# Optimization experiments

Hardware: AMD Instinct MI355X
Metric: run time of the kernel (lower is better)

## Reference

```python
import jax, jax.numpy as jnp
import numpy as np

D_MODEL = 1024
BATCH = 4
SEQ = 4096


def setup_inputs() -> dict:
    key = jax.random.key(0)
    kx, kq, kk, kv = jax.random.split(key, 4)
    x = jax.random.normal(kx, (BATCH, SEQ, D_MODEL), dtype=jnp.float32)
    s = 1.0 / np.sqrt(D_MODEL)
    w_q = jax.random.normal(kq, (D_MODEL, D_MODEL), dtype=jnp.float32) * s
    w_k = jax.random.normal(kk, (D_MODEL, D_MODEL), dtype=jnp.float32) * s
    w_v = jax.random.normal(kv, (D_MODEL, D_MODEL), dtype=jnp.float32) * s
    # causal mask: 1 = keep, 0 = masked out (matches torch masked_fill(mask==0, -inf))
    mask = jnp.tril(jnp.ones((SEQ, SEQ), dtype=jnp.int32))
    return {"x": x, "w_q": w_q, "w_k": w_k, "w_v": w_v, "mask": mask}


def reference(x, w_q, w_k, w_v, mask):
    # torch nn.Linear: y = x @ W^T
    q = jnp.einsum("bsd,ed->bse", x, w_q)
    k = jnp.einsum("bsd,ed->bse", x, w_k)
    v = jnp.einsum("bsd,ed->bse", x, w_v)
    scale = 1.0 / jnp.sqrt(jnp.asarray(q.shape[-1], dtype=q.dtype))
    scores = jnp.einsum("bqd,bkd->bqk", q, k) * scale  # [B, S, S]
    scores = jnp.where(mask == 0, -jnp.inf, scores)
    attn = jax.nn.softmax(scores, axis=-1)
    return jnp.einsum("bqk,bkd->bqd", attn, v)
```

## Files before the change

### kernel.cpp

```cpp
#include <hip/hip_runtime.h>
#include <stdint.h>


#define DM   1024
#define SEQ  4096
#define NB   4
#define MTOT (NB * SEQ)

typedef unsigned short u16;
typedef unsigned int u32;
typedef __bf16 bf16x8 __attribute__((ext_vector_type(8)));
typedef float f32x4 __attribute__((ext_vector_type(4)));

__device__ __forceinline__ u16 f2bf(float f) {
    u32 u = __float_as_uint(f);
    u32 r = (u + 0x7fffu + ((u >> 16) & 1u)) >> 16;
    return (u16)r;
}

__device__ __forceinline__ void gl_lds16(const void* gptr, void* lptr) {
    __builtin_amdgcn_global_load_lds(
        (const __attribute__((address_space(1))) void*)gptr,
        (__attribute__((address_space(3))) void*)lptr,
        16, 0, 0);
}

__global__ void cvt_kernel(const float* __restrict__ in, u16* __restrict__ out, int n8) {
    int i = blockIdx.x * 256 + threadIdx.x;
    if (i >= n8) return;
    const float4* p = (const float4*)in + (size_t)i * 2;
    float4 a = p[0], b = p[1];
    uint4 o;
    o.x = (u32)f2bf(a.x) | ((u32)f2bf(a.y) << 16);
    o.y = (u32)f2bf(a.z) | ((u32)f2bf(a.w) << 16);
    o.z = (u32)f2bf(b.x) | ((u32)f2bf(b.y) << 16);
    o.w = (u32)f2bf(b.z) | ((u32)f2bf(b.w) << 16);
    ((uint4*)out)[i] = o;
}

__global__ void zero_kernel(float* __restrict__ p, int n) {
    int i = blockIdx.x * 256 + threadIdx.x;
    if (i < n) p[i] = 0.f;
}

__device__ __forceinline__ void gemm_core(
    const u16* __restrict__ A, int lda,
    const u16* __restrict__ B, int ldb,
    int m0, int n0, int kend,
    u16* sA, u16* sB, f32x4 acc[4][4])
{
    const int tid  = threadIdx.x;
    const int lane = tid & 63;
    const int w    = tid >> 6;
    const int wr   = w >> 1, wc = w & 1;
    const int gi   = lane >> 4, fr = lane & 15;
    const int srow = lane >> 2;
    const int scol = (lane & 3) * 8;

    for (int kt = 0; kt < kend; kt += 32) {
#pragma unroll
        for (int r = 0; r < 2; ++r) {
            int c   = w * 2 + r;
            int row = c * 16 + srow;
            gl_lds16(A + (size_t)(m0 + row) * lda + kt + scol, sA + c * 512 + lane * 8);
            gl_lds16(B + (size_t)(n0 + row) * ldb + kt + scol, sB + c * 512 + lane * 8);
        }
        __syncthreads();
        bf16x8 af[4], bq[4];
#pragma unroll
        for (int mi = 0; mi < 4; ++mi)
            af[mi] = *(const bf16x8*)(sA + (wr * 64 + mi * 16 + fr) * 32 + gi * 8);
#pragma unroll
        for (int ni = 0; ni < 4; ++ni)
            bq[ni] = *(const bf16x8*)(sB + (wc * 64 + ni * 16 + fr) * 32 + gi * 8);
#pragma unroll
        for (int mi = 0; mi < 4; ++mi)
#pragma unroll
            for (int ni = 0; ni < 4; ++ni)
                acc[mi][ni] = __builtin_amdgcn_mfma_f32_16x16x32_bf16(
                    af[mi], bq[ni], acc[mi][ni], 0, 0, 0);
        __syncthreads();
    }
}

__global__ __launch_bounds__(256) void qkv_kernel(
    const u16* __restrict__ xb,
    const u16* __restrict__ wq, const u16* __restrict__ wk, const u16* __restrict__ wv,
    u16* __restrict__ Q, u16* __restrict__ K, u16* __restrict__ Vt)
{
    __shared__ __align__(16) u16 sA[128 * 32];
    __shared__ __align__(16) u16 sB[128 * 32];
    const int nt = blockIdx.x;
    const int mt = blockIdx.y;
    const int which = blockIdx.z;
    const u16* W = which == 0 ? wq : which == 1 ? wk : wv;

    f32x4 acc[4][4];
#pragma unroll
    for (int a = 0; a < 4; ++a)
#pragma unroll
        for (int b = 0; b < 4; ++b) acc[a][b] = f32x4{0.f, 0.f, 0.f, 0.f};

    gemm_core(xb, DM, W, DM, mt * 128, nt * 128, DM, sA, sB, acc);

    const int lane = threadIdx.x & 63;
    const int w = threadIdx.x >> 6, wr = w >> 1, wc = w & 1;
    const int gi = lane >> 4, fr = lane & 15;

    if (which < 2) {
        u16* O = which == 0 ? Q : K;
#pragma unroll
        for (int mi = 0; mi < 4; ++mi)
#pragma unroll
            for (int ni = 0; ni < 4; ++ni)
#pragma unroll
                for (int i = 0; i < 4; ++i) {
                    int gm = mt * 128 + wr * 64 + mi * 16 + gi * 4 + i;
                    int gn = nt * 128 + wc * 64 + ni * 16 + fr;
                    O[(size_t)gm * DM + gn] = f2bf(acc[mi][ni][i]);
                }
    } else {
#pragma unroll
        for (int mi = 0; mi < 4; ++mi)
#pragma unroll
            for (int ni = 0; ni < 4; ++ni) {
                int gm = mt * 128 + wr * 64 + mi * 16 + gi * 4;
                int gn = nt * 128 + wc * 64 + ni * 16 + fr;
                int b = gm >> 12, s = gm & (SEQ - 1);
                uint2 pk;
                pk.x = (u32)f2bf(acc[mi][ni][0]) | ((u32)f2bf(acc[mi][ni][1]) << 16);
                pk.y = (u32)f2bf(acc[mi][ni][2]) | ((u32)f2bf(acc[mi][ni][3]) << 16);
                *(uint2*)(Vt + ((size_t)(b * DM + gn)) * SEQ + s) = pk;
            }
    }
}

__global__ __launch_bounds__(256) void scores_kernel(
    const u16* __restrict__ Q, const u16* __restrict__ K,
    u16* __restrict__ P, float* __restrict__ rowsum, int b0)
{
    const int ktile = blockIdx.x, qtile = blockIdx.y, z = blockIdx.z;
    if (ktile > qtile) return;
    const int b = b0 + z;
    const u16* Qb = Q + (size_t)b * SEQ * DM;
    const u16* Kb = K + (size_t)b * SEQ * DM;
    u16* Pb = P + (size_t)z * SEQ * SEQ;

    __shared__ __align__(16) u16 sA[128 * 32];
    __shared__ __align__(16) u16 sB[128 * 32];
    f32x4 acc[4][4];
#pragma unroll
    for (int a = 0; a < 4; ++a)
#pragma unroll
        for (int c = 0; c < 4; ++c) acc[a][c] = f32x4{0.f, 0.f, 0.f, 0.f};

    gemm_core(Qb, DM, Kb, DM, qtile * 128, ktile * 128, DM, sA, sB, acc);

    const int lane = threadIdx.x & 63;
    const int w = threadIdx.x >> 6, wr = w >> 1, wc = w & 1;
    const int gi = lane >> 4, fr = lane & 15;
    const int qt0 = qtile * 128, kt0 = ktile * 128;

#pragma unroll
    for (int mi = 0; mi < 4; ++mi) {
        float rs[4] = {0.f, 0.f, 0.f, 0.f};
#pragma unroll
        for (int ni = 0; ni < 4; ++ni)
#pragma unroll
            for (int i = 0; i < 4; ++i) {
                int gq = qt0 + wr * 64 + mi * 16 + gi * 4 + i;
                int gk = kt0 + wc * 64 + ni * 16 + fr;
                float p = (gk <= gq) ? __expf(acc[mi][ni][i] * 0.03125f) : 0.f;
                Pb[(size_t)gq * SEQ + gk] = f2bf(p);
                rs[i] += p;
            }
#pragma unroll
        for (int i = 0; i < 4; ++i) {
            float s = rs[i];
            s += __shfl_xor(s, 1);
            s += __shfl_xor(s, 2);
            s += __shfl_xor(s, 4);
            s += __shfl_xor(s, 8);
            if (fr == 0) {
                int gq = qt0 + wr * 64 + mi * 16 + gi * 4 + i;
                atomicAdd(&rowsum[(size_t)b * SEQ + gq], s);
            }
        }
    }
}

__global__ __launch_bounds__(256) void pv_kernel(
    const u16* __restrict__ P, const u16* __restrict__ Vt,
    const float* __restrict__ rowsum, float* __restrict__ out, int b0)
{
    const int et = blockIdx.x;
    const int qt = 31 - (int)blockIdx.y;
    const int z = blockIdx.z;
    const int b = b0 + z;
    const u16* Pb = P + (size_t)z * SEQ * SEQ;
    const u16* Vb = Vt + (size_t)b * DM * SEQ;

    __shared__ __align__(16) u16 sA[128 * 32];
    __shared__ __align__(16) u16 sB[128 * 32];
    f32x4 acc[4][4];
#pragma unroll
    for (int a = 0; a < 4; ++a)
#pragma unroll
        for (int c = 0; c < 4; ++c) acc[a][c] = f32x4{0.f, 0.f, 0.f, 0.f};

    const int kend = (qt + 1) * 128;
    gemm_core(Pb, SEQ, Vb, SEQ, qt * 128, et * 128, kend, sA, sB, acc);

    const int lane = threadIdx.x & 63;
    const int w = threadIdx.x >> 6, wr = w >> 1, wc = w & 1;
    const int gi = lane >> 4, fr = lane & 15;

#pragma unroll
    for (int mi = 0; mi < 4; ++mi)
#pragma unroll
        for (int i = 0; i < 4; ++i) {
            int gq = qt * 128 + wr * 64 + mi * 16 + gi * 4 + i;
            float inv = 1.0f / rowsum[(size_t)b * SEQ + gq];
#pragma unroll
            for (int ni = 0; ni < 4; ++ni) {
                int ge = et * 128 + wc * 64 + ni * 16 + fr;
                out[((size_t)b * SEQ + gq) * DM + ge] = acc[mi][ni][i] * inv;
            }
        }
}

extern "C" void kernel_launch(void* const* d_in, const int* in_sizes, int n_in,
                              void* d_out, int out_size, void* d_ws, size_t ws_size,
                              hipStream_t stream)
{
    const float* x  = (const float*)d_in[0];
    const float* wq = (const float*)d_in[1];
    const float* wk = (const float*)d_in[2];
    const float* wv = (const float*)d_in[3];
    float* out = (float*)d_out;
    char* ws = (char*)d_ws;
    const size_t MB = 1u << 20;

    auto need = [&](int g) {
        return (size_t)(32 * g + 96 + 6) * MB + (size_t)(NB * SEQ * 4) + 65536;
    };
    int g = (ws_size >= need(4)) ? 4 : (ws_size >= need(2)) ? 2 : 1;

    size_t off = 0;
    u16* P  = (u16*)(ws);            off += (size_t)32 * MB * g;
    u16* xb = (u16*)(ws);
    u16* Q  = (u16*)(ws + off);      off += 32 * MB;
    u16* K  = (u16*)(ws + off);      off += 32 * MB;
    u16* Vt = (u16*)(ws + off);      off += 32 * MB;
    u16* wqb = (u16*)(ws + off);     off += 2 * MB;
    u16* wkb = (u16*)(ws + off);     off += 2 * MB;
    u16* wvb = (u16*)(ws + off);     off += 2 * MB;
    float* rowsum = (float*)(ws + off);

    cvt_kernel<<<(MTOT * DM / 8) / 256, 256, 0, stream>>>(x, xb, MTOT * DM / 8);
    cvt_kernel<<<(DM * DM / 8) / 256, 256, 0, stream>>>(wq, wqb, DM * DM / 8);
    cvt_kernel<<<(DM * DM / 8) / 256, 256, 0, stream>>>(wk, wkb, DM * DM / 8);
    cvt_kernel<<<(DM * DM / 8) / 256, 256, 0, stream>>>(wv, wvb, DM * DM / 8);
    zero_kernel<<<(NB * SEQ) / 256, 256, 0, stream>>>(rowsum, NB * SEQ);

    qkv_kernel<<<dim3(8, 128, 3), 256, 0, stream>>>(xb, wqb, wkb, wvb, Q, K, Vt);

    for (int b0 = 0; b0 < NB; b0 += g) {
        scores_kernel<<<dim3(32, 32, g), 256, 0, stream>>>(Q, K, P, rowsum, b0);
        pv_kernel<<<dim3(8, 32, g), 256, 0, stream>>>(P, Vt, rowsum, out, b0);
    }
}
```

Before: 604.3 us.

## Use 128x256 triple-buffered GEMM tiles, triangular scores grid, split-K PV with combine

Replaces the 128x128 single-buffered GEMM core with a 512-thread 128x256 tile, triple-buffered LDS staging with XOR swizzle, and fine-grained vmcnt waits instead of double syncthreads per k-step. The scores kernel now launches only lower-triangular tiles via a linear index, and the PV kernel splits the longest causal rows into two K halves through a balanced item table, with a combine kernel to sum and normalize. The goal is better data reuse, load/compute overlap, and load balance across the causal triangle. It costs an extra 32MB workspace buffer and a combine pass, plus more LDS per block.

```diff
diff --git a/kernel.cpp b/kernel.cpp
--- a/kernel.cpp
+++ b/kernel.cpp
@@ -6,6 +6,9 @@
 #define SEQ  4096
 #define NB   4
 #define MTOT (NB * SEQ)
+
+#define SLOT_U16 12288
+#define LDS_U16  36864
 
 typedef unsigned short u16;
 typedef unsigned int u32;
@@ -43,68 +46,87 @@
     if (i < n) p[i] = 0.f;
 }
 
-__device__ __forceinline__ void gemm_core(
-    const u16* __restrict__ A, int lda,
-    const u16* __restrict__ B, int ldb,
-    int m0, int n0, int kend,
-    u16* sA, u16* sB, f32x4 acc[4][4])
-{
+__device__ __forceinline__ void stage_tile(const u16* __restrict__ A, int lda, int m0,
+                                           const u16* __restrict__ B, int ldb, int n0,
+                                           int kt, u16* slot, int tid) {
+    int row  = tid >> 2;
+    int csrc = (((tid & 3) ^ (row & 3)) << 3);
+    gl_lds16(A + (size_t)(m0 + row) * lda + kt * 32 + csrc,       slot + tid * 8);
+    gl_lds16(B + (size_t)(n0 + row) * ldb + kt * 32 + csrc,       slot + 4096 + tid * 8);
+    gl_lds16(B + (size_t)(n0 + 128 + row) * ldb + kt * 32 + csrc, slot + 8192 + tid * 8);
+}
+
+__device__ __forceinline__ void gemm128x256(const u16* __restrict__ A, int lda,
+                                            const u16* __restrict__ B, int ldb,
+                                            int m0, int n0, int NT,
+                                            u16* lds, f32x4 acc[4][4]) {
     const int tid  = threadIdx.x;
     const int lane = tid & 63;
     const int w    = tid >> 6;
-    const int wr   = w >> 1, wc = w & 1;
+    const int wr   = w >> 2, wc = w & 3;
     const int gi   = lane >> 4, fr = lane & 15;
-    const int srow = lane >> 2;
-    const int scol = (lane & 3) * 8;
-
-    for (int kt = 0; kt < kend; kt += 32) {
-#pragma unroll
-        for (int r = 0; r < 2; ++r) {
-            int c   = w * 2 + r;
-            int row = c * 16 + srow;
-            gl_lds16(A + (size_t)(m0 + row) * lda + kt + scol, sA + c * 512 + lane * 8);
-            gl_lds16(B + (size_t)(n0 + row) * ldb + kt + scol, sB + c * 512 + lane * 8);
-        }
-        __syncthreads();
+    const int cx   = (gi * 16) ^ ((fr & 3) << 4);
+    const int rA   = wr * 64 + fr;
+    const int rB   = wc * 64 + fr;
+
+    u16 *sc = lds, *sn1 = lds + SLOT_U16, *sn2 = lds + 2 * SLOT_U16;
+
+    stage_tile(A, lda, m0, B, ldb, n0, 0, sc, tid);
+    if (NT > 1) stage_tile(A, lda, m0, B, ldb, n0, 1, sn1, tid);
+    asm volatile("s_waitcnt vmcnt(3)" ::: "memory");
+    __builtin_amdgcn_sched_barrier(0);
+    __builtin_amdgcn_s_barrier();
+
+    for (int t = 0; t < NT; ++t) {
+        if (t + 2 < NT) stage_tile(A, lda, m0, B, ldb, n0, t + 2, sn2, tid);
+
+        const char* sb = (const char*)sc;
         bf16x8 af[4], bq[4];
 #pragma unroll
         for (int mi = 0; mi < 4; ++mi)
-            af[mi] = *(const bf16x8*)(sA + (wr * 64 + mi * 16 + fr) * 32 + gi * 8);
+            af[mi] = *(const bf16x8*)(sb + (rA + mi * 16) * 64 + cx);
 #pragma unroll
         for (int ni = 0; ni < 4; ++ni)
-            bq[ni] = *(const bf16x8*)(sB + (wc * 64 + ni * 16 + fr) * 32 + gi * 8);
+            bq[ni] = *(const bf16x8*)(sb + 8192 + (rB + ni * 16) * 64 + cx);
 #pragma unroll
         for (int mi = 0; mi < 4; ++mi)
 #pragma unroll
             for (int ni = 0; ni < 4; ++ni)
                 acc[mi][ni] = __builtin_amdgcn_mfma_f32_16x16x32_bf16(
                     af[mi], bq[ni], acc[mi][ni], 0, 0, 0);
-        __syncthreads();
+
+        if (t + 1 < NT) {
+            if (t + 2 < NT) { asm volatile("s_waitcnt vmcnt(3)" ::: "memory"); }
+            else            { asm volatile("s_waitcnt vmcnt(0)" ::: "memory"); }
+            __builtin_amdgcn_sched_barrier(0);
+            __builtin_amdgcn_s_barrier();
+        }
+        u16* tmp = sc; sc = sn1; sn1 = sn2; sn2 = tmp;
     }
 }
 
-__global__ __launch_bounds__(256) void qkv_kernel(
+#define ACC_INIT(acc)                                                        \
+    _Pragma("unroll") for (int a_ = 0; a_ < 4; ++a_)                         \
+    _Pragma("unroll") for (int b_ = 0; b_ < 4; ++b_)                         \
+        acc[a_][b_] = f32x4{0.f, 0.f, 0.f, 0.f};
+
+__global__ __launch_bounds__(512, 2) void qkv_kernel(
     const u16* __restrict__ xb,
     const u16* __restrict__ wq, const u16* __restrict__ wk, const u16* __restrict__ wv,
     u16* __restrict__ Q, u16* __restrict__ K, u16* __restrict__ Vt)
 {
-    __shared__ __align__(16) u16 sA[128 * 32];
-    __shared__ __align__(16) u16 sB[128 * 32];
+    __shared__ __align__(16) u16 lds[LDS_U16];
     const int nt = blockIdx.x;
     const int mt = blockIdx.y;
     const int which = blockIdx.z;
     const u16* W = which == 0 ? wq : which == 1 ? wk : wv;
 
     f32x4 acc[4][4];
-#pragma unroll
-    for (int a = 0; a < 4; ++a)
-#pragma unroll
-        for (int b = 0; b < 4; ++b) acc[a][b] = f32x4{0.f, 0.f, 0.f, 0.f};
-
-    gemm_core(xb, DM, W, DM, mt * 128, nt * 128, DM, sA, sB, acc);
+    ACC_INIT(acc);
+    gemm128x256(xb, DM, W, DM, mt * 128, nt * 256, DM / 32, lds, acc);
 
     const int lane = threadIdx.x & 63;
-    const int w = threadIdx.x >> 6, wr = w >> 1, wc = w & 1;
+    const int w = threadIdx.x >> 6, wr = w >> 2, wc = w & 3;
     const int gi = lane >> 4, fr = lane & 15;
 
     if (which < 2) {
@@ -116,7 +138,7 @@
 #pragma unroll
                 for (int i = 0; i < 4; ++i) {
                     int gm = mt * 128 + wr * 64 + mi * 16 + gi * 4 + i;
-                    int gn = nt * 128 + wc * 64 + ni * 16 + fr;
+                    int gn = nt * 256 + wc * 64 + ni * 16 + fr;
                     O[(size_t)gm * DM + gn] = f2bf(acc[mi][ni][i]);
                 }
     } else {
@@ -125,7 +147,7 @@
 #pragma unroll
             for (int ni = 0; ni < 4; ++ni) {
                 int gm = mt * 128 + wr * 64 + mi * 16 + gi * 4;
-                int gn = nt * 128 + wc * 64 + ni * 16 + fr;
+                int gn = nt * 256 + wc * 64 + ni * 16 + fr;
                 int b = gm >> 12, s = gm & (SEQ - 1);
                 uint2 pk;
                 pk.x = (u32)f2bf(acc[mi][ni][0]) | ((u32)f2bf(acc[mi][ni][1]) << 16);
@@ -135,31 +157,28 @@
     }
 }
 
-__global__ __launch_bounds__(256) void scores_kernel(
+__global__ __launch_bounds__(512, 2) void scores_kernel(
     const u16* __restrict__ Q, const u16* __restrict__ K,
     u16* __restrict__ P, float* __restrict__ rowsum, int b0)
 {
-    const int ktile = blockIdx.x, qtile = blockIdx.y, z = blockIdx.z;
-    if (ktile > qtile) return;
+    int rem = blockIdx.x, qi = 0;
+    while (rem >= (qi >> 1) + 1) { rem -= (qi >> 1) + 1; qi++; }
+    const int kt = rem;
+    const int z = blockIdx.z;
     const int b = b0 + z;
     const u16* Qb = Q + (size_t)b * SEQ * DM;
     const u16* Kb = K + (size_t)b * SEQ * DM;
     u16* Pb = P + (size_t)z * SEQ * SEQ;
 
-    __shared__ __align__(16) u16 sA[128 * 32];
-    __shared__ __align__(16) u16 sB[128 * 32];
+    __shared__ __align__(16) u16 lds[LDS_U16];
     f32x4 acc[4][4];
-#pragma unroll
-    for (int a = 0; a < 4; ++a)
-#pragma unroll
-        for (int c = 0; c < 4; ++c) acc[a][c] = f32x4{0.f, 0.f, 0.f, 0.f};
-
-    gemm_core(Qb, DM, Kb, DM, qtile * 128, ktile * 128, DM, sA, sB, acc);
+    ACC_INIT(acc);
+    gemm128x256(Qb, DM, Kb, DM, qi * 128, kt * 256, DM / 32, lds, acc);
 
     const int lane = threadIdx.x & 63;
-    const int w = threadIdx.x >> 6, wr = w >> 1, wc = w & 1;
+    const int w = threadIdx.x >> 6, wr = w >> 2, wc = w & 3;
     const int gi = lane >> 4, fr = lane & 15;
-    const int qt0 = qtile * 128, kt0 = ktile * 128;
+    const int qt0 = qi * 128, kt0 = kt * 256;
 
 #pragma unroll
     for (int mi = 0; mi < 4; ++mi) {
@@ -189,44 +208,97 @@
     }
 }
 
-__global__ __launch_bounds__(256) void pv_kernel(
+#define PVI(qi, h, s) ((u16)((qi) | ((h) << 8) | ((s) << 9)))
+__device__ const u16 pv_items[48] = {
+    PVI(15,0,0), PVI(31,0,1), PVI(31,1,1),
+    PVI(30,0,1), PVI(30,1,1),
+    PVI(14,0,0), PVI(29,0,1), PVI(29,1,1),
+    PVI(28,0,1), PVI(28,1,1),
+    PVI(13,0,0), PVI(27,0,1), PVI(27,1,1),
+    PVI(26,0,1), PVI(26,1,1),
+    PVI(12,0,0), PVI(25,0,1), PVI(25,1,1),
+    PVI(24,0,1), PVI(24,1,1),
+    PVI(11,0,0), PVI(23,0,1), PVI(23,1,1),
+    PVI(22,0,1), PVI(22,1,1),
+    PVI(10,0,0), PVI(21,0,1), PVI(21,1,1),
+    PVI(20,0,1), PVI(20,1,1),
+    PVI( 9,0,0), PVI(19,0,1), PVI(19,1,1),
+    PVI(18,0,1), PVI(18,1,1),
+    PVI( 8,0,0), PVI(17,0,1), PVI(17,1,1),
+    PVI(16,0,1), PVI(16,1,1),
+    PVI( 7,0,0), PVI( 6,0,0), PVI( 5,0,0), PVI( 4,0,0),
+    PVI( 3,0,0), PVI( 2,0,0), PVI( 1,0,0), PVI( 0,0,0)
+};
+
+__global__ __launch_bounds__(512, 2) void pv_kernel(
     const u16* __restrict__ P, const u16* __restrict__ Vt,
-    const float* __restrict__ rowsum, float* __restrict__ out, int b0)
+    const float* __restrict__ rowsum, float* __restrict__ out,
+    float* __restrict__ part, int b0, int gshift, int mode)
 {
-    const int et = blockIdx.x;
-    const int qt = 31 - (int)blockIdx.y;
-    const int z = blockIdx.z;
+    const int x = blockIdx.x;
+    const int item = x >> gshift;
+    const int z = x & ((1 << gshift) - 1);
+    const int et = blockIdx.y;
+    int qi, half, split;
+    if (mode) { u16 v = pv_items[item]; qi = v & 255 & 63; half = (v >> 8) & 1; split = (v >> 9) & 1; }
+    else      { qi = 31 - item; half = 0; split = 0; }
     const int b = b0 + z;
     const u16* Pb = P + (size_t)z * SEQ * SEQ;
     const u16* Vb = Vt + (size_t)b * DM * SEQ;
 
-    __shared__ __align__(16) u16 sA[128 * 32];
-    __shared__ __align__(16) u16 sB[128 * 32];
+    int NT;
+    size_t koff;
+    if (split) { NT = 2 * (qi + 1); koff = (size_t)(half ? 2 * (qi + 1) : 0) * 32; }
+    else       { NT = 4 * (qi + 1); koff = 0; }
+
+    __shared__ __align__(16) u16 lds[LDS_U16];
     f32x4 acc[4][4];
-#pragma unroll
-    for (int a = 0; a < 4; ++a)
-#pragma unroll
-        for (int c = 0; c < 4; ++c) acc[a][c] = f32x4{0.f, 0.f, 0.f, 0.f};
-
-    const int kend = (qt + 1) * 128;
-    gemm_core(Pb, SEQ, Vb, SEQ, qt * 128, et * 128, kend, sA, sB, acc);
+    ACC_INIT(acc);
+    gemm128x256(Pb + koff, SEQ, Vb + koff, SEQ, qi * 128, et * 256, NT, lds, acc);
 
     const int lane = threadIdx.x & 63;
-    const int w = threadIdx.x >> 6, wr = w >> 1, wc = w & 1;
+    const int w = threadIdx.x >> 6, wr = w >> 2, wc = w & 3;
     const int gi = lane >> 4, fr = lane & 15;
 
 #pragma unroll
     for (int mi = 0; mi < 4; ++mi)
 #pragma unroll
         for (int i = 0; i < 4; ++i) {
-            int gq = qt * 128 + wr * 64 + mi * 16 + gi * 4 + i;
-            float inv = 1.0f / rowsum[(size_t)b * SEQ + gq];
+            int gq = qi * 128 + wr * 64 + mi * 16 + gi * 4 + i;
 #pragma unroll
             for (int ni = 0; ni < 4; ++ni) {
-                int ge = et * 128 + wc * 64 + ni * 16 + fr;
-                out[((size_t)b * SEQ + gq) * DM + ge] = acc[mi][ni][i] * inv;
+                int ge = et * 256 + wc * 64 + ni * 16 + fr;
+                float v = acc[mi][ni][i];
+                if (!split) {
+                    float inv = 1.0f / rowsum[(size_t)b * SEQ + gq];
+                    out[((size_t)b * SEQ + gq) * DM + ge] = v * inv;
+                } else if (half == 0) {
+                    out[((size_t)b * SEQ + gq) * DM + ge] = v;
+                } else {
+                    part[((size_t)b * 2048 + (gq - 2048)) * DM + ge] = v;
+                }
             }
         }
+}
+
+__global__ void combine_kernel(float* __restrict__ out, const float* __restrict__ part,
+                               const float* __restrict__ rowsum) {
+    int i = blockIdx.x * 256 + threadIdx.x;
+    int e4 = i & 255;
+    int r  = (i >> 8) & 2047;
+    int b  = i >> 19;
+    int gq = r + 2048;
+    float inv = 1.0f / rowsum[(size_t)b * SEQ + gq];
+    size_t oi = ((size_t)b * SEQ + gq) * 256 + e4;
+    size_t pi = ((size_t)b * 2048 + r) * 256 + e4;
+    float4 o = ((const float4*)out)[oi];
+    float4 p = ((const float4*)part)[pi];
+    float4 rlt;
+    rlt.x = (o.x + p.x) * inv;
+    rlt.y = (o.y + p.y) * inv;
+    rlt.z = (o.z + p.z) * inv;
+    rlt.w = (o.w + p.w) * inv;
+    ((float4*)out)[oi] = rlt;
 }
 
 extern "C" void kernel_launch(void* const* d_in, const int* in_sizes, int n_in,
@@ -241,10 +313,18 @@
     char* ws = (char*)d_ws;
     const size_t MB = 1u << 20;
 
-    auto need = [&](int g) {
-        return (size_t)(32 * g + 96 + 6) * MB + (size_t)(NB * SEQ * 4) + 65536;
+    auto need = [&](int g, int split) {
+        return (size_t)(32 * g + 96 + 6 + (split ? 32 : 0)) * MB
+               + (size_t)(NB * SEQ * 4) + 65536;
     };
-    int g = (ws_size >= need(4)) ? 4 : (ws_size >= need(2)) ? 2 : 1;
+    int g, do_split;
+    if      (ws_size >= need(4, 1)) { g = 4; do_split = 1; }
+    else if (ws_size >= need(2, 1)) { g = 2; do_split = 1; }
+    else if (ws_size >= need(1, 1)) { g = 1; do_split = 1; }
+    else if (ws_size >= need(4, 0)) { g = 4; do_split = 0; }
+    else if (ws_size >= need(2, 0)) { g = 2; do_split = 0; }
+    else                            { g = 1; do_split = 0; }
+    const int gshift = (g == 4) ? 2 : (g == 2) ? 1 : 0;
 
     size_t off = 0;
     u16* P  = (u16*)(ws);            off += (size_t)32 * MB * g;
@@ -255,6 +335,7 @@
     u16* wqb = (u16*)(ws + off);     off += 2 * MB;
     u16* wkb = (u16*)(ws + off);     off += 2 * MB;
     u16* wvb = (u16*)(ws + off);     off += 2 * MB;
+    float* part = (float*)(ws + off); if (do_split) off += 32 * MB;
     float* rowsum = (float*)(ws + off);
 
     cvt_kernel<<<(MTOT * DM / 8) / 256, 256, 0, stream>>>(x, xb, MTOT * DM / 8);
@@ -263,10 +344,14 @@
     cvt_kernel<<<(DM * DM / 8) / 256, 256, 0, stream>>>(wv, wvb, DM * DM / 8);
     zero_kernel<<<(NB * SEQ) / 256, 256, 0, stream>>>(rowsum, NB * SEQ);
 
-    qkv_kernel<<<dim3(8, 128, 3), 256, 0, stream>>>(xb, wqb, wkb, wvb, Q, K, Vt);
-
+    qkv_kernel<<<dim3(4, 128, 3), 512, 0, stream>>>(xb, wqb, wkb, wvb, Q, K, Vt);
+
+    const int nitems = do_split ? 48 : 32;
     for (int b0 = 0; b0 < NB; b0 += g) {
-        scores_kernel<<<dim3(32, 32, g), 256, 0, stream>>>(Q, K, P, rowsum, b0);
-        pv_kernel<<<dim3(8, 32, g), 256, 0, stream>>>(P, Vt, rowsum, out, b0);
+        scores_kernel<<<dim3(272, 1, g), 512, 0, stream>>>(Q, K, P, rowsum, b0);
+        pv_kernel<<<dim3(nitems * g, 4, 1), 512, 0, stream>>>(
+            P, Vt, rowsum, out, part, b0, gshift, do_split);
     }
-}
+    if (do_split)
+        combine_kernel<<<8192, 256, 0, stream>>>(out, part, rowsum);
+}
```

New measurement: 560.4 us. 7.3% less time.
